# Kernel optimization log

Hardware: AMD Instinct MI355X
Metric: run time of the kernel (lower is better)

Reference implementation:

```python
import jax, jax.numpy as jnp
import numpy as np

B, L, D, C = 32, 2048, 1024, 1024  # batch, max_length, input_size, context_size


def setup_inputs() -> dict:
    key = jax.random.key(0)
    ks = jax.random.split(key, 4)
    sequence = jax.random.normal(ks[0], (B, L, D), dtype=jnp.float32)
    query = jax.random.normal(ks[1], (B, C), dtype=jnp.float32)
    # lengths in [1, L] so every row has at least one unmasked position
    lengths = jax.random.randint(ks[2], (B,), 1, L + 1, dtype=jnp.int32)
    W_h = jax.random.normal(ks[3], (C, D), dtype=jnp.float32) / np.sqrt(D).astype(np.float32)
    b_h = jnp.zeros((C,), dtype=jnp.float32)
    return {"sequence": sequence, "query": query, "lengths": lengths, "W_h": W_h, "b_h": b_h}


def reference(sequence, query, lengths, W_h, b_h):
    # method='general': energies = (W_h @ sequence + b_h) . query
    h = jnp.einsum('bld,cd->blc', sequence, W_h) + b_h          # [B, L, C]
    energies = jnp.einsum('blc,bc->bl', h, query)                # [B, L]
    # sequence_mask(lengths, L): True where position < length
    mask = jnp.arange(energies.shape[1]) < lengths[:, None]      # [B, L]
    # masked_normalization_inf: fill masked positions with -inf, softmax
    masked = jnp.where(mask, energies, -jnp.inf)
    scores = jax.nn.softmax(masked, axis=-1)                     # [B, L]
    contexts = jnp.einsum('bl,bld->bd', scores, sequence)        # [B, D]
    return contexts, scores
```

## Files before the change

kernel.cpp:

```cpp
#include <hip/hip_runtime.h>
#include <math.h>

#define B_ 32
#define L_ 2048
#define D_ 1024
#define C_ 1024
#define CSPLIT 16
#define WROWS 8
#define NWAVE 8
#define BROWS 64
#define NCH (L_ / BROWS)


__global__ __launch_bounds__(256) void k_vpart(const float* __restrict__ q,
                                               const float* __restrict__ W,
                                               float* __restrict__ vpart) {
    int cc = blockIdx.x, dc = blockIdx.y;
    int t  = threadIdx.x;
    __shared__ float qs[B_][65];
    #pragma unroll
    for (int i = 0; i < 8; ++i) {
        int idx = t + i * 256;
        int b = idx >> 6, cl = idx & 63;
        qs[b][cl] = q[b * C_ + cc * 64 + cl];
    }
    __syncthreads();

    int dl4 = t & 15;
    int bg  = t >> 4;
    float4 a0 = {0,0,0,0}, a1 = {0,0,0,0};
    const float4* W4 = reinterpret_cast<const float4*>(W);
    for (int c = 0; c < 64; ++c) {
        float4 w = W4[(size_t)(cc * 64 + c) * (D_ / 4) + dc * 16 + dl4];
        float q0 = qs[bg * 2 + 0][c];
        float q1 = qs[bg * 2 + 1][c];
        a0.x = fmaf(q0, w.x, a0.x); a0.y = fmaf(q0, w.y, a0.y);
        a0.z = fmaf(q0, w.z, a0.z); a0.w = fmaf(q0, w.w, a0.w);
        a1.x = fmaf(q1, w.x, a1.x); a1.y = fmaf(q1, w.y, a1.y);
        a1.z = fmaf(q1, w.z, a1.z); a1.w = fmaf(q1, w.w, a1.w);
    }
    size_t base = ((size_t)cc * B_ + bg * 2) * D_ + dc * 64 + dl4 * 4;
    *reinterpret_cast<float4*>(vpart + base)      = a0;
    *reinterpret_cast<float4*>(vpart + base + D_) = a1;
}

__global__ __launch_bounds__(256) void k_vreduce(const float* __restrict__ vpart,
                                                 float* __restrict__ v,
                                                 const float* __restrict__ q,
                                                 const float* __restrict__ bh,
                                                 float* __restrict__ cb) {
    int b = blockIdx.x, dq = blockIdx.y, t = threadIdx.x;
    int d = dq * 256 + t;
    float a = 0.f;
    #pragma unroll
    for (int cc = 0; cc < CSPLIT; ++cc)
        a += vpart[((size_t)cc * B_ + b) * D_ + d];
    v[(size_t)b * D_ + d] = a;

    if (dq == 0) {
        float s = 0.f;
        for (int c = t; c < C_; c += 256) s += bh[c] * q[b * C_ + c];
        __shared__ float red[256];
        red[t] = s; __syncthreads();
        for (int off = 128; off > 0; off >>= 1) {
            if (t < off) red[t] += red[t + off];
            __syncthreads();
        }
        if (t == 0) cb[b] = red[0];
    }
}

__global__ __launch_bounds__(512) void k_fused(const float* __restrict__ seq,
                                               const float* __restrict__ v,
                                               const float* __restrict__ cb,
                                               const int* __restrict__ lenp,
                                               float* __restrict__ energ,
                                               float* __restrict__ pm,
                                               float* __restrict__ ps,
                                               float* __restrict__ pc) {
    int b  = blockIdx.y;
    int ch = blockIdx.x;
    int len = lenp[b];
    int l0 = ch * BROWS;
    if (l0 >= len) return;
    int t = threadIdx.x, wid = t >> 6, lane = t & 63;
    int lw0 = l0 + wid * WROWS;

    const float* vb = v + (size_t)b * D_;
    float4 v0 = *reinterpret_cast<const float4*>(vb +       lane * 4);
    float4 v1 = *reinterpret_cast<const float4*>(vb + 256 + lane * 4);
    float4 v2 = *reinterpret_cast<const float4*>(vb + 512 + lane * 4);
    float4 v3 = *reinterpret_cast<const float4*>(vb + 768 + lane * 4);
    float cbb = cb[b];

    float m = -INFINITY, s = 0.f;
    float c[16];
    #pragma unroll
    for (int i = 0; i < 16; ++i) c[i] = 0.f;

    __shared__ float e_sm[BROWS];
    __shared__ float lm[NWAVE], ls[NWAVE];
    __shared__ float lc[NWAVE][D_];

    auto process = [&](const float4& s0, const float4& s1,
                       const float4& s2, const float4& s3, int r) {
        float ac0 = 0.f, ac1 = 0.f, ac2 = 0.f, ac3 = 0.f;
        ac0 = fmaf(s0.x, v0.x, ac0); ac0 = fmaf(s0.y, v0.y, ac0);
        ac0 = fmaf(s0.z, v0.z, ac0); ac0 = fmaf(s0.w, v0.w, ac0);
        ac1 = fmaf(s1.x, v1.x, ac1); ac1 = fmaf(s1.y, v1.y, ac1);
        ac1 = fmaf(s1.z, v1.z, ac1); ac1 = fmaf(s1.w, v1.w, ac1);
        ac2 = fmaf(s2.x, v2.x, ac2); ac2 = fmaf(s2.y, v2.y, ac2);
        ac2 = fmaf(s2.z, v2.z, ac2); ac2 = fmaf(s2.w, v2.w, ac2);
        ac3 = fmaf(s3.x, v3.x, ac3); ac3 = fmaf(s3.y, v3.y, ac3);
        ac3 = fmaf(s3.z, v3.z, ac3); ac3 = fmaf(s3.w, v3.w, ac3);
        float acc = (ac0 + ac1) + (ac2 + ac3);
        #pragma unroll
        for (int off = 32; off; off >>= 1) acc += __shfl_xor(acc, off);
        float e = acc + cbb;
        if (lane == 0) e_sm[wid * WROWS + r] = e;
        if (e > m) {
            float sc = __expf(m - e);
            s = fmaf(s, sc, 1.f);
            c[ 0] = fmaf(c[ 0], sc, s0.x); c[ 1] = fmaf(c[ 1], sc, s0.y);
            c[ 2] = fmaf(c[ 2], sc, s0.z); c[ 3] = fmaf(c[ 3], sc, s0.w);
            c[ 4] = fmaf(c[ 4], sc, s1.x); c[ 5] = fmaf(c[ 5], sc, s1.y);
            c[ 6] = fmaf(c[ 6], sc, s1.z); c[ 7] = fmaf(c[ 7], sc, s1.w);
            c[ 8] = fmaf(c[ 8], sc, s2.x); c[ 9] = fmaf(c[ 9], sc, s2.y);
            c[10] = fmaf(c[10], sc, s2.z); c[11] = fmaf(c[11], sc, s2.w);
            c[12] = fmaf(c[12], sc, s3.x); c[13] = fmaf(c[13], sc, s3.y);
            c[14] = fmaf(c[14], sc, s3.z); c[15] = fmaf(c[15], sc, s3.w);
            m = e;
        } else {
            float p = __expf(e - m);
            s += p;
            c[ 0] = fmaf(p, s0.x, c[ 0]); c[ 1] = fmaf(p, s0.y, c[ 1]);
            c[ 2] = fmaf(p, s0.z, c[ 2]); c[ 3] = fmaf(p, s0.w, c[ 3]);
            c[ 4] = fmaf(p, s1.x, c[ 4]); c[ 5] = fmaf(p, s1.y, c[ 5]);
            c[ 6] = fmaf(p, s1.z, c[ 6]); c[ 7] = fmaf(p, s1.w, c[ 7]);
            c[ 8] = fmaf(p, s2.x, c[ 8]); c[ 9] = fmaf(p, s2.y, c[ 9]);
            c[10] = fmaf(p, s2.z, c[10]); c[11] = fmaf(p, s2.w, c[11]);
            c[12] = fmaf(p, s3.x, c[12]); c[13] = fmaf(p, s3.y, c[13]);
            c[14] = fmaf(p, s3.z, c[14]); c[15] = fmaf(p, s3.w, c[15]);
        }
    };

    int nr = (lw0 < len) ? min(WROWS, len - lw0) : 0;
    if (nr > 0) {
        const float* rowp = seq + ((size_t)b * L_ + lw0) * D_;
        float4 cs0 = *reinterpret_cast<const float4*>(rowp +       lane * 4);
        float4 cs1 = *reinterpret_cast<const float4*>(rowp + 256 + lane * 4);
        float4 cs2 = *reinterpret_cast<const float4*>(rowp + 512 + lane * 4);
        float4 cs3 = *reinterpret_cast<const float4*>(rowp + 768 + lane * 4);
        for (int r = 0; r < nr - 1; ++r) {
            const float* nrow = rowp + (size_t)(r + 1) * D_;
            float4 ns0 = *reinterpret_cast<const float4*>(nrow +       lane * 4);
            float4 ns1 = *reinterpret_cast<const float4*>(nrow + 256 + lane * 4);
            float4 ns2 = *reinterpret_cast<const float4*>(nrow + 512 + lane * 4);
            float4 ns3 = *reinterpret_cast<const float4*>(nrow + 768 + lane * 4);
            process(cs0, cs1, cs2, cs3, r);
            cs0 = ns0; cs1 = ns1; cs2 = ns2; cs3 = ns3;
        }
        process(cs0, cs1, cs2, cs3, nr - 1);
    }

    {
        float4 w0 = {c[ 0], c[ 1], c[ 2], c[ 3]};
        float4 w1 = {c[ 4], c[ 5], c[ 6], c[ 7]};
        float4 w2 = {c[ 8], c[ 9], c[10], c[11]};
        float4 w3 = {c[12], c[13], c[14], c[15]};
        *reinterpret_cast<float4*>(&lc[wid][      lane * 4]) = w0;
        *reinterpret_cast<float4*>(&lc[wid][256 + lane * 4]) = w1;
        *reinterpret_cast<float4*>(&lc[wid][512 + lane * 4]) = w2;
        *reinterpret_cast<float4*>(&lc[wid][768 + lane * 4]) = w3;
        if (lane == 0) { lm[wid] = m; ls[wid] = s; }
    }
    __syncthreads();

    if (t < BROWS) energ[(size_t)b * L_ + l0 + t] = e_sm[t];

    float mb = lm[0];
    #pragma unroll
    for (int i = 1; i < NWAVE; ++i) mb = fmaxf(mb, lm[i]);
    float wgt[NWAVE], sb = 0.f;
    #pragma unroll
    for (int i = 0; i < NWAVE; ++i) {
        wgt[i] = (lm[i] == mb) ? 1.f : __expf(lm[i] - mb);
        sb = fmaf(wgt[i], ls[i], sb);
    }

    float ox = 0.f, oy = 0.f;
    #pragma unroll
    for (int i = 0; i < NWAVE; ++i) {
        ox = fmaf(wgt[i], lc[i][t * 2],     ox);
        oy = fmaf(wgt[i], lc[i][t * 2 + 1], oy);
    }
    size_t pidx = (size_t)b * NCH + ch;
    if (t == 0) { pm[pidx] = mb; ps[pidx] = sb; }
    float2 o2 = {ox, oy};
    *reinterpret_cast<float2*>(pc + pidx * D_ + t * 2) = o2;
}

__global__ __launch_bounds__(256) void k_final(const float* __restrict__ pm,
                                               const float* __restrict__ ps,
                                               const float* __restrict__ pc,
                                               const float* __restrict__ energ,
                                               const int* __restrict__ lenp,
                                               float* __restrict__ ctx,
                                               float* __restrict__ scores) {
    int b = blockIdx.x, sl = blockIdx.y, t = threadIdx.x;
    int len = lenp[b];
    int nch = (len + BROWS - 1) / BROWS;
    __shared__ float wgt[NCH];
    __shared__ float Msh, Ssh;
    if (t < 64) {
        float mi = (t < nch) ? pm[(size_t)b * NCH + t] : -INFINITY;
        float si = (t < nch) ? ps[(size_t)b * NCH + t] : 0.f;
        float M = mi;
        #pragma unroll
        for (int off = 32; off; off >>= 1) M = fmaxf(M, __shfl_xor(M, off));
        float ew = (t < nch) ? __expf(mi - M) : 0.f;
        float S  = ew * si;
        #pragma unroll
        for (int off = 32; off; off >>= 1) S += __shfl_xor(S, off);
        if (t < nch) wgt[t] = ew / S;
        if (t == 0) { Msh = M; Ssh = S; }
    }
    __syncthreads();
    float M = Msh;
    float invS = 1.f / Ssh;

    if (t < 128) {
        int d = sl * 128 + t;
        float o = 0.f;
        for (int ch = 0; ch < nch; ++ch)
            o = fmaf(wgt[ch], pc[((size_t)b * NCH + ch) * D_ + d], o);
        ctx[(size_t)b * D_ + d] = o;
    }

    int l = sl * 256 + t;
    float e = energ[(size_t)b * L_ + l];
    scores[(size_t)b * L_ + l] = (l < len) ? __expf(e - M) * invS : 0.f;
}

extern "C" void kernel_launch(void* const* d_in, const int* in_sizes, int n_in,
                              void* d_out, int out_size, void* d_ws, size_t ws_size,
                              hipStream_t stream) {
    const float* seq     = (const float*)d_in[0];
    const float* query   = (const float*)d_in[1];
    const int*   lengths = (const int*)  d_in[2];
    const float* W_h     = (const float*)d_in[3];
    const float* b_h     = (const float*)d_in[4];

    float* out    = (float*)d_out;
    float* ctx    = out;
    float* scores = out + B_ * D_;

    float* ws    = (float*)d_ws;
    float* v     = ws;
    float* cb    = ws + 32768;
    float* energ = ws + 32800;
    float* vpart = ws + 98336;
    float* pm    = ws + 622624;
    float* ps    = ws + 623648;
    float* pc    = ws + 624672;

    k_vpart  <<<dim3(16, 16), 256, 0, stream>>>(query, W_h, vpart);
    k_vreduce<<<dim3(B_, 4), 256, 0, stream>>>(vpart, v, query, b_h, cb);
    k_fused  <<<dim3(NCH, B_), 512, 0, stream>>>(seq, v, cb, lengths, energ, pm, ps, pc);
    k_final  <<<dim3(B_, 8), 256, 0, stream>>>(pm, ps, pc, energ, lengths, ctx, scores);
}
```

Measured before the change: 45.78 us.

## Fuse query-projection partial and reduce kernels into one per-batch kernel

```diff
diff --git a/kernel.cpp b/kernel.cpp
--- a/kernel.cpp
+++ b/kernel.cpp
@@ -5,68 +5,53 @@
 #define L_ 2048
 #define D_ 1024
 #define C_ 1024
-#define CSPLIT 16
 #define WROWS 8
 #define NWAVE 8
 #define BROWS 64
 #define NCH (L_ / BROWS)
 
 
-__global__ __launch_bounds__(256) void k_vpart(const float* __restrict__ q,
-                                               const float* __restrict__ W,
-                                               float* __restrict__ vpart) {
-    int cc = blockIdx.x, dc = blockIdx.y;
-    int t  = threadIdx.x;
-    __shared__ float qs[B_][65];
-    #pragma unroll
-    for (int i = 0; i < 8; ++i) {
-        int idx = t + i * 256;
-        int b = idx >> 6, cl = idx & 63;
-        qs[b][cl] = q[b * C_ + cc * 64 + cl];
-    }
-    __syncthreads();
-
-    int dl4 = t & 15;
-    int bg  = t >> 4;
-    float4 a0 = {0,0,0,0}, a1 = {0,0,0,0};
-    const float4* W4 = reinterpret_cast<const float4*>(W);
-    for (int c = 0; c < 64; ++c) {
-        float4 w = W4[(size_t)(cc * 64 + c) * (D_ / 4) + dc * 16 + dl4];
-        float q0 = qs[bg * 2 + 0][c];
-        float q1 = qs[bg * 2 + 1][c];
-        a0.x = fmaf(q0, w.x, a0.x); a0.y = fmaf(q0, w.y, a0.y);
-        a0.z = fmaf(q0, w.z, a0.z); a0.w = fmaf(q0, w.w, a0.w);
-        a1.x = fmaf(q1, w.x, a1.x); a1.y = fmaf(q1, w.y, a1.y);
-        a1.z = fmaf(q1, w.z, a1.z); a1.w = fmaf(q1, w.w, a1.w);
-    }
-    size_t base = ((size_t)cc * B_ + bg * 2) * D_ + dc * 64 + dl4 * 4;
-    *reinterpret_cast<float4*>(vpart + base)      = a0;
-    *reinterpret_cast<float4*>(vpart + base + D_) = a1;
-}
-
-__global__ __launch_bounds__(256) void k_vreduce(const float* __restrict__ vpart,
-                                                 float* __restrict__ v,
-                                                 const float* __restrict__ q,
-                                                 const float* __restrict__ bh,
-                                                 float* __restrict__ cb) {
-    int b = blockIdx.x, dq = blockIdx.y, t = threadIdx.x;
-    int d = dq * 256 + t;
-    float a = 0.f;
-    #pragma unroll
-    for (int cc = 0; cc < CSPLIT; ++cc)
-        a += vpart[((size_t)cc * B_ + b) * D_ + d];
-    v[(size_t)b * D_ + d] = a;
-
-    if (dq == 0) {
+__global__ __launch_bounds__(256) void k_v(const float* __restrict__ q,
+                                           const float* __restrict__ W,
+                                           const float* __restrict__ bh,
+                                           float* __restrict__ v,
+                                           float* __restrict__ cb) {
+    int b = blockIdx.x, dc = blockIdx.y;
+    int t = threadIdx.x, w = t >> 6, lane = t & 63;
+    __shared__ float qs[C_];
+    __shared__ float red[3][64];
+    reinterpret_cast<float4*>(qs)[t] =
+        reinterpret_cast<const float4*>(q + (size_t)b * C_)[t];
+    __syncthreads();
+
+    int d  = dc * 64 + lane;
+    int c0 = w * 256;
+    const float* Wp = W + (size_t)c0 * D_ + d;
+    const float* qp = qs + c0;
+    float a0 = 0.f, a1 = 0.f, a2 = 0.f, a3 = 0.f;
+    float a4 = 0.f, a5 = 0.f, a6 = 0.f, a7 = 0.f;
+    for (int i = 0; i < 256; i += 8) {
+        a0 = fmaf(qp[i + 0], Wp[(size_t)(i + 0) * D_], a0);
+        a1 = fmaf(qp[i + 1], Wp[(size_t)(i + 1) * D_], a1);
+        a2 = fmaf(qp[i + 2], Wp[(size_t)(i + 2) * D_], a2);
+        a3 = fmaf(qp[i + 3], Wp[(size_t)(i + 3) * D_], a3);
+        a4 = fmaf(qp[i + 4], Wp[(size_t)(i + 4) * D_], a4);
+        a5 = fmaf(qp[i + 5], Wp[(size_t)(i + 5) * D_], a5);
+        a6 = fmaf(qp[i + 6], Wp[(size_t)(i + 6) * D_], a6);
+        a7 = fmaf(qp[i + 7], Wp[(size_t)(i + 7) * D_], a7);
+    }
+    float a = ((a0 + a1) + (a2 + a3)) + ((a4 + a5) + (a6 + a7));
+    if (w) red[w - 1][lane] = a;
+    __syncthreads();
+    if (w == 0)
+        v[(size_t)b * D_ + d] = a + red[0][lane] + red[1][lane] + red[2][lane];
+
+    if (dc == 0 && w == 3) {
         float s = 0.f;
-        for (int c = t; c < C_; c += 256) s += bh[c] * q[b * C_ + c];
-        __shared__ float red[256];
-        red[t] = s; __syncthreads();
-        for (int off = 128; off > 0; off >>= 1) {
-            if (t < off) red[t] += red[t + off];
-            __syncthreads();
-        }
-        if (t == 0) cb[b] = red[0];
+        for (int c = lane; c < C_; c += 64) s = fmaf(bh[c], qs[c], s);
+        #pragma unroll
+        for (int off = 32; off; off >>= 1) s += __shfl_xor(s, off);
+        if (lane == 0) cb[b] = s;
     }
 }
 
@@ -259,13 +244,11 @@
     float* v     = ws;
     float* cb    = ws + 32768;
     float* energ = ws + 32800;
-    float* vpart = ws + 98336;
     float* pm    = ws + 622624;
     float* ps    = ws + 623648;
     float* pc    = ws + 624672;
 
-    k_vpart  <<<dim3(16, 16), 256, 0, stream>>>(query, W_h, vpart);
-    k_vreduce<<<dim3(B_, 4), 256, 0, stream>>>(vpart, v, query, b_h, cb);
-    k_fused  <<<dim3(NCH, B_), 512, 0, stream>>>(seq, v, cb, lengths, energ, pm, ps, pc);
-    k_final  <<<dim3(B_, 8), 256, 0, stream>>>(pm, ps, pc, energ, lengths, ctx, scores);
-}
+    k_v    <<<dim3(B_, 16), 256, 0, stream>>>(query, W_h, b_h, v, cb);
+    k_fused<<<dim3(NCH, B_), 512, 0, stream>>>(seq, v, cb, lengths, energ, pm, ps, pc);
+    k_final<<<dim3(B_, 8), 256, 0, stream>>>(pm, ps, pc, energ, lengths, ctx, scores);
+}
```

New measurement: 48.41 us. +5.7%, slower.
